# Performance work log

Measured on AMD Instinct MI355X. Metric: run time of the kernel, lower is better.

The kernel has to match this reference:

```python
import jax, jax.numpy as jnp
import numpy as np
from jax import lax

RES = [8, 12, 20, 18, 32]
C = 4            # n_features
NCELLS = 2
DOMAIN = (0.0, 1.0, 0.0, 1.0)
NPTS = 1000000


def depthwise_conv3x3(a, w):
    # a: (Ncells, C, R, R); w: (C, 1, 3, 3) depthwise (groups=C), padding=1, no bias
    return lax.conv_general_dilated(
        a, w, window_strides=(1, 1), padding='SAME',
        dimension_numbers=('NCHW', 'OIHW', 'NCHW'), feature_group_count=C)


def grid_sample_2d(feat, gx, gy):
    # Custom bilinear grid sample with per-cell half-cell offsets (offset=True).
    # feat: (Ncells, C, IH, IW); gx, gy: (N,) normalized coords in [-1, 1].
    n_cells, c, ih, iw = feat.shape
    ix = (gx + 1.0) * 0.5 * (iw - 1)          # pixel coords, align_corners=True
    iy = (gy + 1.0) * 0.5 * (ih - 1)
    off = jnp.arange(n_cells, dtype=feat.dtype) / n_cells  # staggered cells
    ix = ix[None, :] + off[:, None]            # (Ncells, N)
    iy = iy[None, :] + off[:, None]
    ix0 = jnp.floor(ix)
    iy0 = jnp.floor(iy)
    wx = ix - ix0                              # fractional weights (unclamped)
    wy = iy - iy0
    x0 = jnp.clip(ix0.astype(jnp.int32), 0, iw - 1)
    x1 = jnp.clip(ix0.astype(jnp.int32) + 1, 0, iw - 1)
    y0 = jnp.clip(iy0.astype(jnp.int32), 0, ih - 1)
    y1 = jnp.clip(iy0.astype(jnp.int32) + 1, 0, ih - 1)
    flat = feat.reshape(n_cells, c, ih * iw)

    def gather(yy, xx):
        idx = yy * iw + xx                      # (Ncells, N)
        return jnp.take_along_axis(flat, idx[:, None, :], axis=2)  # (Ncells, C, N)

    nw = gather(y0, x0)
    ne = gather(y0, x1)
    sw = gather(y1, x0)
    se = gather(y1, x1)
    w_nw = ((1 - wx) * (1 - wy))[:, None, :]
    w_ne = (wx * (1 - wy))[:, None, :]
    w_sw = ((1 - wx) * wy)[:, None, :]
    w_se = (wx * wy)[:, None, :]
    return nw * w_nw + ne * w_ne + sw * w_sw + se * w_se  # (Ncells, C, N)


def encode_level(alpha, conv_w, gx, gy):
    a = jnp.tanh(depthwise_conv3x3(alpha, conv_w))
    s = grid_sample_2d(a, gx, gy)               # (Ncells, C, N)
    return s.sum(0).T                           # (N, C) == F.sum(0).view(C,-1).t()


def setup_inputs() -> dict:
    key = jax.random.key(0)
    kx, ky, kw = jax.random.split(key, 3)
    inp = {
        'x': jax.random.uniform(kx, (NPTS, 1), dtype=jnp.float32),
        'y': jax.random.uniform(ky, (NPTS, 1), dtype=jnp.float32),
        'conv_w': jax.random.normal(kw, (C, 1, 3, 3), dtype=jnp.float32) * 0.3,
    }
    for i, r in enumerate(RES):
        inp[f'F{i}'] = jax.random.uniform(
            jax.random.fold_in(key, i + 10), (NCELLS, C, r, r),
            dtype=jnp.float32, minval=-1e-5, maxval=1e-5)
    return inp


def reference(x, y, F0, F1, F2, F3, F4, conv_w):
    x_min, x_max, y_min, y_max = DOMAIN
    gx = ((x - x_min) / (x_max - x_min)) * 2.0 - 1.0   # (N,1)
    gy = ((y - y_min) / (y_max - y_min)) * 2.0 - 1.0
    gx = gx[:, 0]
    gy = gy[:, 0]
    feats = [encode_level(F, conv_w, gx, gy) for F in (F0, F1, F2, F3, F4)]
    return jnp.concatenate(feats, axis=1)              # (N, 5*C)
```

## Files before the change

### kernel.cpp

```cpp
#include <hip/hip_runtime.h>
#include <hip/hip_fp16.h>
#include <cmath>


#define NTH 512
#define PPT 4

typedef _Float16 half4 __attribute__((ext_vector_type(4)));

#define OFF0 0
#define OFF1 648
#define OFF2 2000
#define OFF3 5528
#define OFF4 8416
#define TOTH 17128
#define TOTV (TOTH / 8)

template<int R>
__device__ __forceinline__ void conv_level(const float* __restrict__ F,
                                           const float* __restrict__ w,
                                           _Float16* __restrict__ dst,
                                           int tid, int nth)
{
    constexpr int P = R + 1;
    const int n = 8 * P * P;
    for (int i = tid; i < n; i += nth) {
        int c    = i & 3;
        int pos  = i >> 2;
        int cell = (pos >= P * P) ? 1 : 0;
        int rem  = pos - cell * P * P;
        int yy   = rem / P;
        int xx   = rem - yy * P;
        int ys   = min(yy, R - 1);
        int xs   = min(xx, R - 1);
        const float* Fc = F + (cell * 4 + c) * R * R;
        float acc = 0.f;
#pragma unroll
        for (int ky = 0; ky < 3; ++ky) {
#pragma unroll
            for (int kx = 0; kx < 3; ++kx) {
                int sy = ys + ky - 1, sx = xs + kx - 1;
                if ((unsigned)sy < (unsigned)R && (unsigned)sx < (unsigned)R)
                    acc += w[c * 9 + ky * 3 + kx] * Fc[sy * R + sx];
            }
        }
        dst[(cell * P * P + yy * P + xx) * 4 + c] =
            (_Float16)(tanhf(acc) * 1024.0f);
    }
}

__global__ void conv_kernel(const float* __restrict__ F0, const float* __restrict__ F1,
                            const float* __restrict__ F2, const float* __restrict__ F3,
                            const float* __restrict__ F4, const float* __restrict__ w,
                            _Float16* __restrict__ tab)
{
    int tid = blockIdx.x * blockDim.x + threadIdx.x;
    int nth = gridDim.x * blockDim.x;
    conv_level<8 >(F0, w, tab + OFF0, tid, nth);
    conv_level<12>(F1, w, tab + OFF1, tid, nth);
    conv_level<20>(F2, w, tab + OFF2, tid, nth);
    conv_level<18>(F3, w, tab + OFF3, tid, nth);
    conv_level<32>(F4, w, tab + OFF4, tid, nth);
}

template<int R>
__device__ __forceinline__ float4 sample_level(const _Float16* __restrict__ lt,
                                               float px, float py)
{
    constexpr int P = R + 1;
    float fx = px * (float)(R - 1);
    float fy = py * (float)(R - 1);
    float4 acc = make_float4(0.f, 0.f, 0.f, 0.f);
#pragma unroll
    for (int cell = 0; cell < 2; ++cell) {
        float ixc = cell ? fx + 0.5f : fx;
        float iyc = cell ? fy + 0.5f : fy;
        float fx0 = floorf(ixc);
        float fy0 = floorf(iyc);
        float wx = ixc - fx0;
        float wy = iyc - fy0;
        int x0 = (int)fx0;
        int y0 = (int)fy0;
        const half4* cb = (const half4*)lt + (cell * P * P + y0 * P + x0);
        half4 nw = cb[0];
        half4 ne = cb[1];
        half4 sw = cb[P];
        half4 se = cb[P + 1];
        float u = 1.f - wx, v = 1.f - wy;
        float wnw = u * v, wne = wx * v, wsw = u * wy, wse = wx * wy;
        acc.x = fmaf(wnw, (float)nw[0], acc.x); acc.x = fmaf(wne, (float)ne[0], acc.x);
        acc.x = fmaf(wsw, (float)sw[0], acc.x); acc.x = fmaf(wse, (float)se[0], acc.x);
        acc.y = fmaf(wnw, (float)nw[1], acc.y); acc.y = fmaf(wne, (float)ne[1], acc.y);
        acc.y = fmaf(wsw, (float)sw[1], acc.y); acc.y = fmaf(wse, (float)se[1], acc.y);
        acc.z = fmaf(wnw, (float)nw[2], acc.z); acc.z = fmaf(wne, (float)ne[2], acc.z);
        acc.z = fmaf(wsw, (float)sw[2], acc.z); acc.z = fmaf(wse, (float)se[2], acc.z);
        acc.w = fmaf(wnw, (float)nw[3], acc.w); acc.w = fmaf(wne, (float)ne[3], acc.w);
        acc.w = fmaf(wsw, (float)sw[3], acc.w); acc.w = fmaf(wse, (float)se[3], acc.w);
    }
    return acc;
}

__device__ __forceinline__ void sample_body(const _Float16* lds,
                                            const float* __restrict__ x,
                                            const float* __restrict__ y,
                                            float* __restrict__ out, int npts)
{
    int p0 = blockIdx.x * (NTH * PPT) + threadIdx.x;
    float pxs[PPT], pys[PPT];
#pragma unroll
    for (int k = 0; k < PPT; ++k) {
        int p = p0 + k * NTH;
        int pc = (p < npts) ? p : 0;
        pxs[k] = x[pc];
        pys[k] = y[pc];
    }
    const float s = 0.0009765625f;
    for (int k = 0; k < PPT; ++k) {
        int p = p0 + k * NTH;
        float px = pxs[k];
        float py = pys[k];
        float4 r0 = sample_level<8 >(lds + OFF0, px, py);
        float4 r1 = sample_level<12>(lds + OFF1, px, py);
        float4 r2 = sample_level<20>(lds + OFF2, px, py);
        float4 r3 = sample_level<18>(lds + OFF3, px, py);
        float4 r4 = sample_level<32>(lds + OFF4, px, py);
        if (p < npts) {
            r0.x *= s; r0.y *= s; r0.z *= s; r0.w *= s;
            r1.x *= s; r1.y *= s; r1.z *= s; r1.w *= s;
            r2.x *= s; r2.y *= s; r2.z *= s; r2.w *= s;
            r3.x *= s; r3.y *= s; r3.z *= s; r3.w *= s;
            r4.x *= s; r4.y *= s; r4.z *= s; r4.w *= s;
            float4* op = (float4*)(out + (size_t)p * 20);
            op[0] = r0; op[1] = r1; op[2] = r2; op[3] = r3; op[4] = r4;
        }
    }
}

__global__ __launch_bounds__(NTH, 4) void sample_kernel(const float* __restrict__ x,
                                                        const float* __restrict__ y,
                                                        const _Float16* __restrict__ tab,
                                                        float* __restrict__ out, int npts)
{
    __shared__ __align__(16) _Float16 lds[TOTH];
    const uint4* g4 = (const uint4*)tab;
    uint4* l4 = (uint4*)lds;
    for (int i = threadIdx.x; i < TOTV; i += NTH)
        l4[i] = g4[i];
    __syncthreads();
    sample_body(lds, x, y, out, npts);
}

__global__ __launch_bounds__(NTH, 4) void fused_kernel(const float* __restrict__ x,
                                                       const float* __restrict__ y,
                                                       const float* __restrict__ F0,
                                                       const float* __restrict__ F1,
                                                       const float* __restrict__ F2,
                                                       const float* __restrict__ F3,
                                                       const float* __restrict__ F4,
                                                       const float* __restrict__ w,
                                                       float* __restrict__ out, int npts)
{
    __shared__ __align__(16) _Float16 lds[TOTH];
    conv_level<8 >(F0, w, lds + OFF0, threadIdx.x, NTH);
    conv_level<12>(F1, w, lds + OFF1, threadIdx.x, NTH);
    conv_level<20>(F2, w, lds + OFF2, threadIdx.x, NTH);
    conv_level<18>(F3, w, lds + OFF3, threadIdx.x, NTH);
    conv_level<32>(F4, w, lds + OFF4, threadIdx.x, NTH);
    __syncthreads();
    sample_body(lds, x, y, out, npts);
}

extern "C" void kernel_launch(void* const* d_in, const int* in_sizes, int n_in,
                              void* d_out, int out_size, void* d_ws, size_t ws_size,
                              hipStream_t stream)
{
    const float* x  = (const float*)d_in[0];
    const float* y  = (const float*)d_in[1];
    const float* w  = (const float*)d_in[2];
    const float* F0 = (const float*)d_in[3];
    const float* F1 = (const float*)d_in[4];
    const float* F2 = (const float*)d_in[5];
    const float* F3 = (const float*)d_in[6];
    const float* F4 = (const float*)d_in[7];
    float* out = (float*)d_out;
    int npts = in_sizes[0];

    int nb = (npts + NTH * PPT - 1) / (NTH * PPT);

    if (ws_size >= (size_t)TOTH * sizeof(_Float16)) {
        _Float16* tab = (_Float16*)d_ws;
        conv_kernel<<<(TOTH + 255) / 256, 256, 0, stream>>>(F0, F1, F2, F3, F4, w, tab);
        sample_kernel<<<nb, NTH, 0, stream>>>(x, y, tab, out, npts);
    } else {
        fused_kernel<<<nb, NTH, 0, stream>>>(x, y, F0, F1, F2, F3, F4, w, out, npts);
    }
}
```

Baseline: 125.1 us.

## Use packed fp32 lerp math, halve points per thread, raise occupancy bound

The sampling math becomes two-component float vectors with lerp-style FMAs, which lets the compiler emit packed FP32 instructions and cuts the per-corner weight arithmetic. Points per thread drop from 4 to 2, the x/y prefetch loop is merged into the compute loop, and the sample kernel's launch-bounds occupancy hint rises from 4 to 6. Together these aim to lower ALU work and register pressure so more waves can hide LDS and store latency. The cost is twice as many blocks, each spending the same effort to copy the table into LDS, and less memory-level parallelism per thread.

Measured after the change: 131.8 us. 1.05x slower.

```diff
diff --git a/kernel.cpp b/kernel.cpp
--- a/kernel.cpp
+++ b/kernel.cpp
@@ -1,12 +1,12 @@
 #include <hip/hip_runtime.h>
-#include <hip/hip_fp16.h>
 #include <cmath>
 
 
 #define NTH 512
-#define PPT 4
+#define PPT 2
 
-typedef _Float16 half4 __attribute__((ext_vector_type(4)));
+typedef float    f32x2 __attribute__((ext_vector_type(2)));
+typedef _Float16 f16x4 __attribute__((ext_vector_type(4)));
 
 #define OFF0 0
 #define OFF1 648
@@ -15,6 +15,8 @@
 #define OFF4 8416
 #define TOTH 17128
 #define TOTV (TOTH / 8)
+
+static __device__ __forceinline__ f32x2 splat2(float a) { return (f32x2){a, a}; }
 
 template<int R>
 __device__ __forceinline__ void conv_level(const float* __restrict__ F,
@@ -64,13 +66,14 @@
 }
 
 template<int R>
-__device__ __forceinline__ float4 sample_level(const _Float16* __restrict__ lt,
-                                               float px, float py)
+__device__ __forceinline__ void sample_level(const _Float16* __restrict__ lt,
+                                             float px, float py,
+                                             f32x2& out_lo, f32x2& out_hi)
 {
     constexpr int P = R + 1;
     float fx = px * (float)(R - 1);
     float fy = py * (float)(R - 1);
-    float4 acc = make_float4(0.f, 0.f, 0.f, 0.f);
+    f32x2 alo = {0.f, 0.f}, ahi = {0.f, 0.f};
 #pragma unroll
     for (int cell = 0; cell < 2; ++cell) {
         float ixc = cell ? fx + 0.5f : fx;
@@ -81,23 +84,25 @@
         float wy = iyc - fy0;
         int x0 = (int)fx0;
         int y0 = (int)fy0;
-        const half4* cb = (const half4*)lt + (cell * P * P + y0 * P + x0);
-        half4 nw = cb[0];
-        half4 ne = cb[1];
-        half4 sw = cb[P];
-        half4 se = cb[P + 1];
-        float u = 1.f - wx, v = 1.f - wy;
-        float wnw = u * v, wne = wx * v, wsw = u * wy, wse = wx * wy;
-        acc.x = fmaf(wnw, (float)nw[0], acc.x); acc.x = fmaf(wne, (float)ne[0], acc.x);
-        acc.x = fmaf(wsw, (float)sw[0], acc.x); acc.x = fmaf(wse, (float)se[0], acc.x);
-        acc.y = fmaf(wnw, (float)nw[1], acc.y); acc.y = fmaf(wne, (float)ne[1], acc.y);
-        acc.y = fmaf(wsw, (float)sw[1], acc.y); acc.y = fmaf(wse, (float)se[1], acc.y);
-        acc.z = fmaf(wnw, (float)nw[2], acc.z); acc.z = fmaf(wne, (float)ne[2], acc.z);
-        acc.z = fmaf(wsw, (float)sw[2], acc.z); acc.z = fmaf(wse, (float)se[2], acc.z);
-        acc.w = fmaf(wnw, (float)nw[3], acc.w); acc.w = fmaf(wne, (float)ne[3], acc.w);
-        acc.w = fmaf(wsw, (float)sw[3], acc.w); acc.w = fmaf(wse, (float)se[3], acc.w);
+        const f16x4* cb = (const f16x4*)lt + (cell * (P * P) + y0 * P + x0);
+        f16x4 nw = cb[0];
+        f16x4 ne = cb[1];
+        f16x4 sw = cb[P];
+        f16x4 se = cb[P + 1];
+        f32x2 nwlo = {(float)nw[0], (float)nw[1]}, nwhi = {(float)nw[2], (float)nw[3]};
+        f32x2 nelo = {(float)ne[0], (float)ne[1]}, nehi = {(float)ne[2], (float)ne[3]};
+        f32x2 swlo = {(float)sw[0], (float)sw[1]}, swhi = {(float)sw[2], (float)sw[3]};
+        f32x2 selo = {(float)se[0], (float)se[1]}, sehi = {(float)se[2], (float)se[3]};
+        f32x2 wx2 = splat2(wx), wy2 = splat2(wy);
+        f32x2 tlo = __builtin_elementwise_fma(wx2, nelo - nwlo, nwlo);
+        f32x2 thi = __builtin_elementwise_fma(wx2, nehi - nwhi, nwhi);
+        f32x2 blo = __builtin_elementwise_fma(wx2, selo - swlo, swlo);
+        f32x2 bhi = __builtin_elementwise_fma(wx2, sehi - swhi, swhi);
+        alo += __builtin_elementwise_fma(wy2, blo - tlo, tlo);
+        ahi += __builtin_elementwise_fma(wy2, bhi - thi, thi);
     }
-    return acc;
+    out_lo = alo;
+    out_hi = ahi;
 }
 
 __device__ __forceinline__ void sample_body(const _Float16* lds,
@@ -106,37 +111,33 @@
                                             float* __restrict__ out, int npts)
 {
     int p0 = blockIdx.x * (NTH * PPT) + threadIdx.x;
-    float pxs[PPT], pys[PPT];
+    const f32x2 s2 = {0.0009765625f, 0.0009765625f};
 #pragma unroll
     for (int k = 0; k < PPT; ++k) {
         int p = p0 + k * NTH;
         int pc = (p < npts) ? p : 0;
-        pxs[k] = x[pc];
-        pys[k] = y[pc];
-    }
-    const float s = 0.0009765625f;
-    for (int k = 0; k < PPT; ++k) {
-        int p = p0 + k * NTH;
-        float px = pxs[k];
-        float py = pys[k];
-        float4 r0 = sample_level<8 >(lds + OFF0, px, py);
-        float4 r1 = sample_level<12>(lds + OFF1, px, py);
-        float4 r2 = sample_level<20>(lds + OFF2, px, py);
-        float4 r3 = sample_level<18>(lds + OFF3, px, py);
-        float4 r4 = sample_level<32>(lds + OFF4, px, py);
+        float px = x[pc];
+        float py = y[pc];
+        f32x2 l0a, l0b, l1a, l1b, l2a, l2b, l3a, l3b, l4a, l4b;
+        sample_level<8 >(lds + OFF0, px, py, l0a, l0b);
+        sample_level<12>(lds + OFF1, px, py, l1a, l1b);
+        sample_level<20>(lds + OFF2, px, py, l2a, l2b);
+        sample_level<18>(lds + OFF3, px, py, l3a, l3b);
+        sample_level<32>(lds + OFF4, px, py, l4a, l4b);
         if (p < npts) {
-            r0.x *= s; r0.y *= s; r0.z *= s; r0.w *= s;
-            r1.x *= s; r1.y *= s; r1.z *= s; r1.w *= s;
-            r2.x *= s; r2.y *= s; r2.z *= s; r2.w *= s;
-            r3.x *= s; r3.y *= s; r3.z *= s; r3.w *= s;
-            r4.x *= s; r4.y *= s; r4.z *= s; r4.w *= s;
+            l0a *= s2; l0b *= s2; l1a *= s2; l1b *= s2; l2a *= s2;
+            l2b *= s2; l3a *= s2; l3b *= s2; l4a *= s2; l4b *= s2;
             float4* op = (float4*)(out + (size_t)p * 20);
-            op[0] = r0; op[1] = r1; op[2] = r2; op[3] = r3; op[4] = r4;
+            op[0] = make_float4(l0a[0], l0a[1], l0b[0], l0b[1]);
+            op[1] = make_float4(l1a[0], l1a[1], l1b[0], l1b[1]);
+            op[2] = make_float4(l2a[0], l2a[1], l2b[0], l2b[1]);
+            op[3] = make_float4(l3a[0], l3a[1], l3b[0], l3b[1]);
+            op[4] = make_float4(l4a[0], l4a[1], l4b[0], l4b[1]);
         }
     }
 }
 
-__global__ __launch_bounds__(NTH, 4) void sample_kernel(const float* __restrict__ x,
+__global__ __launch_bounds__(NTH, 6) void sample_kernel(const float* __restrict__ x,
                                                         const float* __restrict__ y,
                                                         const _Float16* __restrict__ tab,
                                                         float* __restrict__ out, int npts)
```

## Remap lanes to (point, level) pairs for coalesced float4 output stores

Applied to the files above, without the earlier changes.

Each wavefront lane now handles one (point, level) output float4, chosen so that consecutive lanes write consecutive 16-byte chunks of the output. The previous scheme had each thread write five float4s spaced 80 bytes apart. The change is meant to coalesce the dominant global store traffic. In exchange, level parameters become runtime values picked by selects, x/y are loaded redundantly (five times per point), and LDS gathers hit different tables within a wave.

Result: slower. 128.1 us (+2.3%).

```diff
diff --git a/kernel.cpp b/kernel.cpp
--- a/kernel.cpp
+++ b/kernel.cpp
@@ -1,12 +1,11 @@
 #include <hip/hip_runtime.h>
-#include <hip/hip_fp16.h>
 #include <cmath>
 
 
 #define NTH 512
 #define PPT 4
 
-typedef _Float16 half4 __attribute__((ext_vector_type(4)));
+typedef _Float16 f16x4v __attribute__((ext_vector_type(4)));
 
 #define OFF0 0
 #define OFF1 648
@@ -15,6 +14,21 @@
 #define OFF4 8416
 #define TOTH 17128
 #define TOTV (TOTH / 8)
+
+static __device__ __forceinline__ int sel5i(int r, int a, int b, int c, int d, int e) {
+    int v = (r == 1) ? b : a;
+    v = (r == 2) ? c : v;
+    v = (r == 3) ? d : v;
+    v = (r == 4) ? e : v;
+    return v;
+}
+static __device__ __forceinline__ float sel5f(int r, float a, float b, float c, float d, float e) {
+    float v = (r == 1) ? b : a;
+    v = (r == 2) ? c : v;
+    v = (r == 3) ? d : v;
+    v = (r == 4) ? e : v;
+    return v;
+}
 
 template<int R>
 __device__ __forceinline__ void conv_level(const float* __restrict__ F,
@@ -63,14 +77,13 @@
     conv_level<32>(F4, w, tab + OFF4, tid, nth);
 }
 
-template<int R>
-__device__ __forceinline__ float4 sample_level(const _Float16* __restrict__ lt,
-                                               float px, float py)
-{
-    constexpr int P = R + 1;
-    float fx = px * (float)(R - 1);
-    float fy = py * (float)(R - 1);
-    float4 acc = make_float4(0.f, 0.f, 0.f, 0.f);
+__device__ __forceinline__ float4 sample_rt(const _Float16* __restrict__ lt,
+                                            int P, int PP, float rm1,
+                                            float px, float py)
+{
+    float fx = px * rm1;
+    float fy = py * rm1;
+    float ax = 0.f, ay = 0.f, az = 0.f, aw = 0.f;
 #pragma unroll
     for (int cell = 0; cell < 2; ++cell) {
         float ixc = cell ? fx + 0.5f : fx;
@@ -81,23 +94,24 @@
         float wy = iyc - fy0;
         int x0 = (int)fx0;
         int y0 = (int)fy0;
-        const half4* cb = (const half4*)lt + (cell * P * P + y0 * P + x0);
-        half4 nw = cb[0];
-        half4 ne = cb[1];
-        half4 sw = cb[P];
-        half4 se = cb[P + 1];
+        const f16x4v* cb = (const f16x4v*)lt + ((cell ? PP : 0) + y0 * P + x0);
+        f16x4v nw = cb[0];
+        f16x4v ne = cb[1];
+        const f16x4v* cs = cb + P;
+        f16x4v sw = cs[0];
+        f16x4v se = cs[1];
         float u = 1.f - wx, v = 1.f - wy;
         float wnw = u * v, wne = wx * v, wsw = u * wy, wse = wx * wy;
-        acc.x = fmaf(wnw, (float)nw[0], acc.x); acc.x = fmaf(wne, (float)ne[0], acc.x);
-        acc.x = fmaf(wsw, (float)sw[0], acc.x); acc.x = fmaf(wse, (float)se[0], acc.x);
-        acc.y = fmaf(wnw, (float)nw[1], acc.y); acc.y = fmaf(wne, (float)ne[1], acc.y);
-        acc.y = fmaf(wsw, (float)sw[1], acc.y); acc.y = fmaf(wse, (float)se[1], acc.y);
-        acc.z = fmaf(wnw, (float)nw[2], acc.z); acc.z = fmaf(wne, (float)ne[2], acc.z);
-        acc.z = fmaf(wsw, (float)sw[2], acc.z); acc.z = fmaf(wse, (float)se[2], acc.z);
-        acc.w = fmaf(wnw, (float)nw[3], acc.w); acc.w = fmaf(wne, (float)ne[3], acc.w);
-        acc.w = fmaf(wsw, (float)sw[3], acc.w); acc.w = fmaf(wse, (float)se[3], acc.w);
-    }
-    return acc;
+        ax = fmaf(wnw, (float)nw[0], ax); ax = fmaf(wne, (float)ne[0], ax);
+        ax = fmaf(wsw, (float)sw[0], ax); ax = fmaf(wse, (float)se[0], ax);
+        ay = fmaf(wnw, (float)nw[1], ay); ay = fmaf(wne, (float)ne[1], ay);
+        ay = fmaf(wsw, (float)sw[1], ay); ay = fmaf(wse, (float)se[1], ay);
+        az = fmaf(wnw, (float)nw[2], az); az = fmaf(wne, (float)ne[2], az);
+        az = fmaf(wsw, (float)sw[2], az); az = fmaf(wse, (float)se[2], az);
+        aw = fmaf(wnw, (float)nw[3], aw); aw = fmaf(wne, (float)ne[3], aw);
+        aw = fmaf(wsw, (float)sw[3], aw); aw = fmaf(wse, (float)se[3], aw);
+    }
+    return make_float4(ax, ay, az, aw);
 }
 
 __device__ __forceinline__ void sample_body(const _Float16* lds,
@@ -105,33 +119,42 @@
                                             const float* __restrict__ y,
                                             float* __restrict__ out, int npts)
 {
-    int p0 = blockIdx.x * (NTH * PPT) + threadIdx.x;
-    float pxs[PPT], pys[PPT];
+    const int L   = threadIdx.x & 63;
+    const int wid = threadIdx.x >> 6;
+
+    int   dq[5], Pj[5], PPj[5], bas[5];
+    float rm1[5];
+#pragma unroll
+    for (int j = 0; j < 5; ++j) {
+        int g = L + 64 * j;
+        int q = g / 5;
+        int r = g - q * 5;
+        dq[j]  = q;
+        rm1[j] = sel5f(r, 7.f, 11.f, 19.f, 17.f, 31.f);
+        Pj[j]  = sel5i(r, 9, 13, 21, 19, 33);
+        PPj[j] = sel5i(r, 81, 169, 441, 361, 1089);
+        bas[j] = sel5i(r, OFF0, OFF1, OFF2, OFF3, OFF4);
+    }
+
+    float4* out4 = (float4*)out;
+    const int lim4 = npts * 5;
+    const float s = 0.0009765625f;
 #pragma unroll
     for (int k = 0; k < PPT; ++k) {
-        int p = p0 + k * NTH;
-        int pc = (p < npts) ? p : 0;
-        pxs[k] = x[pc];
-        pys[k] = y[pc];
-    }
-    const float s = 0.0009765625f;
-    for (int k = 0; k < PPT; ++k) {
-        int p = p0 + k * NTH;
-        float px = pxs[k];
-        float py = pys[k];
-        float4 r0 = sample_level<8 >(lds + OFF0, px, py);
-        float4 r1 = sample_level<12>(lds + OFF1, px, py);
-        float4 r2 = sample_level<20>(lds + OFF2, px, py);
-        float4 r3 = sample_level<18>(lds + OFF3, px, py);
-        float4 r4 = sample_level<32>(lds + OFF4, px, py);
-        if (p < npts) {
-            r0.x *= s; r0.y *= s; r0.z *= s; r0.w *= s;
-            r1.x *= s; r1.y *= s; r1.z *= s; r1.w *= s;
-            r2.x *= s; r2.y *= s; r2.z *= s; r2.w *= s;
-            r3.x *= s; r3.y *= s; r3.z *= s; r3.w *= s;
-            r4.x *= s; r4.y *= s; r4.z *= s; r4.w *= s;
-            float4* op = (float4*)(out + (size_t)p * 20);
-            op[0] = r0; op[1] = r1; op[2] = r2; op[3] = r3; op[4] = r4;
+        int Wstart = blockIdx.x * (NTH * PPT) + k * NTH + wid * 64;
+        int W5 = Wstart * 5;
+#pragma unroll
+        for (int j = 0; j < 5; ++j) {
+            int qg = Wstart + dq[j];
+            int qc = min(qg, npts - 1);
+            float px = x[qc];
+            float py = y[qc];
+            float4 r4 = sample_rt(lds + bas[j], Pj[j], PPj[j], rm1[j], px, py);
+            int o4 = W5 + L + 64 * j;
+            if (o4 < lim4) {
+                r4.x *= s; r4.y *= s; r4.z *= s; r4.w *= s;
+                out4[o4] = r4;
+            }
         }
     }
 }
```
